# Performance work log

Hardware: AMD Instinct MI355X
Metric: run time of the kernel (lower is better)

## Reference

```python
import jax, jax.numpy as jnp
import numpy as np

N_NODES = 100000
N_EDGES = 1600000
IN_DIM, HID_DIM, LAT_DIM = 128, 128, 32


def gcn_conv(x, W, b, src, dst, ew, num_nodes):
    """PyG GCNConv with improved=True (self-loop fill value 2.0),
    symmetric normalization D^-1/2 (A + 2I) D^-1/2, then linear + bias."""
    loop = jnp.arange(num_nodes)
    src2 = jnp.concatenate([src, loop])
    dst2 = jnp.concatenate([dst, loop])
    ew2 = jnp.concatenate([ew, jnp.full((num_nodes,), 2.0, dtype=x.dtype)])
    # deg[i] = sum of incoming edge weights (incl. self loop weight 2)
    deg = jax.ops.segment_sum(ew2, dst2, num_segments=num_nodes)
    dinv = jnp.where(deg > 0, jax.lax.rsqrt(deg), 0.0)
    norm = dinv[src2] * ew2 * dinv[dst2]           # [E+N]
    h = x @ W                                      # linear first: [N, out]
    msg = h[src2] * norm[:, None]                  # gather + scale: [E+N, out]
    out = jax.ops.segment_sum(msg, dst2, num_segments=num_nodes)
    return out + b


def setup_inputs() -> dict:
    key = jax.random.key(0)
    ks = jax.random.split(key, 8)
    x = jax.random.normal(ks[0], (N_NODES, IN_DIM), dtype=jnp.float32)
    edge_index = jax.random.randint(ks[1], (2, N_EDGES), 0, N_NODES, dtype=jnp.int64)
    edge_weight = jnp.ones((N_EDGES,), dtype=jnp.float32)
    s = 1.0 / np.sqrt(IN_DIM)
    W1 = jax.random.normal(ks[2], (IN_DIM, HID_DIM), dtype=jnp.float32) * s
    b1 = jnp.zeros((HID_DIM,), dtype=jnp.float32)
    sh = 1.0 / np.sqrt(HID_DIM)
    Wm = jax.random.normal(ks[3], (HID_DIM, LAT_DIM), dtype=jnp.float32) * sh
    bm = jnp.zeros((LAT_DIM,), dtype=jnp.float32)
    Ws = jax.random.normal(ks[4], (HID_DIM, LAT_DIM), dtype=jnp.float32) * sh
    bs = jnp.zeros((LAT_DIM,), dtype=jnp.float32)
    return {"x": x, "edge_index": edge_index, "edge_weight": edge_weight,
            "W1": W1, "b1": b1, "Wm": Wm, "bm": bm, "Ws": Ws, "bs": bs}


def reference(x, edge_index, edge_weight, W1, b1, Wm, bm, Ws, bs):
    src, dst = edge_index[0], edge_index[1]
    n = x.shape[0]
    h = gcn_conv(x, W1, b1, src, dst, edge_weight, n)
    h = jax.nn.relu(h)
    z_mean = gcn_conv(h, Wm, bm, src, dst, edge_weight, n)
    z_logstd = gcn_conv(h, Ws, bs, src, dst, edge_weight, n)
    return (z_mean, z_logstd)
```

## Files before the change

### kernel.cpp

```cpp
#include <hip/hip_runtime.h>


#define DIM 128
#define LAT 32
#define SCAN_ELEMS 1024
#define CPAD 32

typedef short bf16x8 __attribute__((ext_vector_type(8)));
typedef float f32x4 __attribute__((ext_vector_type(4)));

__device__ __forceinline__ unsigned short f2bf(float f) {
    unsigned u = __float_as_uint(f);
    return (unsigned short)((u + 0x7fffu + ((u >> 16) & 1u)) >> 16);
}
__device__ __forceinline__ unsigned packbf(float a, float b) {
    return (unsigned)f2bf(a) | ((unsigned)f2bf(b) << 16);
}
__device__ __forceinline__ float2 bfp2f(unsigned u) {
    float2 r;
    r.x = __uint_as_float(u << 16);
    r.y = __uint_as_float(u & 0xffff0000u);
    return r;
}

__global__ void k_x2bf(const float* __restrict__ x, uint2* __restrict__ xb, int n4) {
    int i = blockIdx.x * blockDim.x + threadIdx.x;
    if (i < n4) {
        float4 v = reinterpret_cast<const float4*>(x)[i];
        xb[i] = make_uint2(packbf(v.x, v.y), packbf(v.z, v.w));
    }
}

__global__ void k_rank(const int* __restrict__ dst, int* __restrict__ cursorPad,
                       unsigned short* __restrict__ rank, int E) {
    int e = blockIdx.x * blockDim.x + threadIdx.x;
    if (e < E) rank[e] = (unsigned short)atomicAdd(&cursorPad[(size_t)dst[e] * CPAD], 1);
}

__global__ __launch_bounds__(256) void k_scan1(const int* __restrict__ countsPad,
                                               int* __restrict__ rowptr,
                                               int* __restrict__ bsums, int N) {
    __shared__ int sdata[256];
    const int t = threadIdx.x;
    const int base = blockIdx.x * SCAN_ELEMS + t * 4;
    int v[4];
#pragma unroll
    for (int j = 0; j < 4; ++j) {
        int idx = base + j;
        v[j] = (idx < N) ? countsPad[(size_t)idx * CPAD] : 0;
    }
    int tot = v[0] + v[1] + v[2] + v[3];
    sdata[t] = tot;
    __syncthreads();
    for (int off = 1; off < 256; off <<= 1) {
        int x = 0;
        if (t >= off) x = sdata[t - off];
        __syncthreads();
        if (t >= off) sdata[t] += x;
        __syncthreads();
    }
    int running = sdata[t] - tot;
#pragma unroll
    for (int j = 0; j < 4; ++j) {
        int idx = base + j;
        if (idx < N) rowptr[idx] = running;
        running += v[j];
    }
    if (t == 255) bsums[blockIdx.x] = sdata[255];
}

__global__ void k_scan2(int* __restrict__ bsums, int* __restrict__ rowptr, int NB, int N, int E) {
    int running = 0;
    for (int b = 0; b < NB; ++b) {
        int t = bsums[b];
        bsums[b] = running;
        running += t;
    }
    rowptr[N] = E;
}

__global__ void k_scan3(int* __restrict__ rowptr, const int* __restrict__ bsums, int N) {
    int i = blockIdx.x * blockDim.x + threadIdx.x;
    if (i < N) rowptr[i] += bsums[i >> 10];
}

__global__ void k_place(const int* __restrict__ src, const int* __restrict__ dst,
                        const float* __restrict__ ew, const unsigned short* __restrict__ rank,
                        const int* __restrict__ rowptr, int2* __restrict__ csr, int E) {
    int e = blockIdx.x * blockDim.x + threadIdx.x;
    if (e < E)
        csr[rowptr[dst[e]] + rank[e]] = make_int2(src[e], __float_as_int(ew[e]));
}

__global__ void k_degseg(const int2* __restrict__ csr, const int* __restrict__ rowptr,
                         float* __restrict__ dinv, int N) {
    int i = blockIdx.x * blockDim.x + threadIdx.x;
    if (i >= N) return;
    float deg = 2.0f;
    int p = rowptr[i], end = rowptr[i + 1];
    for (; p < end; ++p) deg += __int_as_float(csr[p].y);
    dinv[i] = (deg > 0.0f) ? rsqrtf(deg) : 0.0f;
}

__global__ void k_prep_w(const float* __restrict__ W1, const float* __restrict__ Wm,
                         const float* __restrict__ Ws, unsigned short* __restrict__ w1t,
                         unsigned short* __restrict__ wct) {
    int i = blockIdx.x * 256 + threadIdx.x;
    if (i < DIM * DIM) {
        int c = i >> 7, k = i & 127;
        w1t[c * DIM + k] = f2bf(W1[k * DIM + c]);
    }
    i -= DIM * DIM;
    if (i >= 0 && i < 64 * DIM) {
        int c = i >> 7, k = i & 127;
        wct[c * DIM + k] = f2bf((c < LAT) ? Wm[k * LAT + c] : Ws[k * LAT + (c - LAT)]);
    }
}

__global__ __launch_bounds__(256) void k_gather128(const int2* __restrict__ csr,
                                                   const int* __restrict__ rowptr,
                                                   const float* __restrict__ dinv,
                                                   const uint4* __restrict__ xb,
                                                   uint4* __restrict__ axb, int N) {
    int node = (blockIdx.x * 256 + threadIdx.x) >> 6;
    int lane = threadIdx.x & 63;
    if (node >= N) return;
    const int q = lane >> 4;
    const int l = lane & 15;
    float di = dinv[node];
    float acc[8];
#pragma unroll
    for (int j = 0; j < 8; ++j) acc[j] = 0.f;
    if (q == 0) {
        uint4 sv = xb[(size_t)node * 16 + l];
        float sl = 2.0f * di;
        float2 s0 = bfp2f(sv.x), s1 = bfp2f(sv.y), s2 = bfp2f(sv.z), s3 = bfp2f(sv.w);
        acc[0] = s0.x * sl; acc[1] = s0.y * sl;
        acc[2] = s1.x * sl; acc[3] = s1.y * sl;
        acc[4] = s2.x * sl; acc[5] = s2.y * sl;
        acc[6] = s3.x * sl; acc[7] = s3.y * sl;
    }
    int p = rowptr[node] + q;
    int end = rowptr[node + 1];
    for (; p + 4 < end; p += 8) {
        int2 e0 = csr[p];
        int2 e1 = csr[p + 4];
        float n0 = __int_as_float(e0.y) * dinv[e0.x];
        float n1 = __int_as_float(e1.y) * dinv[e1.x];
        uint4 u0 = xb[(size_t)e0.x * 16 + l];
        uint4 u1 = xb[(size_t)e1.x * 16 + l];
        float2 a0 = bfp2f(u0.x), a1 = bfp2f(u0.y), a2 = bfp2f(u0.z), a3 = bfp2f(u0.w);
        acc[0] = fmaf(a0.x, n0, acc[0]); acc[1] = fmaf(a0.y, n0, acc[1]);
        acc[2] = fmaf(a1.x, n0, acc[2]); acc[3] = fmaf(a1.y, n0, acc[3]);
        acc[4] = fmaf(a2.x, n0, acc[4]); acc[5] = fmaf(a2.y, n0, acc[5]);
        acc[6] = fmaf(a3.x, n0, acc[6]); acc[7] = fmaf(a3.y, n0, acc[7]);
        float2 b0 = bfp2f(u1.x), b1 = bfp2f(u1.y), b2 = bfp2f(u1.z), b3 = bfp2f(u1.w);
        acc[0] = fmaf(b0.x, n1, acc[0]); acc[1] = fmaf(b0.y, n1, acc[1]);
        acc[2] = fmaf(b1.x, n1, acc[2]); acc[3] = fmaf(b1.y, n1, acc[3]);
        acc[4] = fmaf(b2.x, n1, acc[4]); acc[5] = fmaf(b2.y, n1, acc[5]);
        acc[6] = fmaf(b3.x, n1, acc[6]); acc[7] = fmaf(b3.y, n1, acc[7]);
    }
    if (p < end) {
        int2 e0 = csr[p];
        float n0 = __int_as_float(e0.y) * dinv[e0.x];
        uint4 u0 = xb[(size_t)e0.x * 16 + l];
        float2 a0 = bfp2f(u0.x), a1 = bfp2f(u0.y), a2 = bfp2f(u0.z), a3 = bfp2f(u0.w);
        acc[0] = fmaf(a0.x, n0, acc[0]); acc[1] = fmaf(a0.y, n0, acc[1]);
        acc[2] = fmaf(a1.x, n0, acc[2]); acc[3] = fmaf(a1.y, n0, acc[3]);
        acc[4] = fmaf(a2.x, n0, acc[4]); acc[5] = fmaf(a2.y, n0, acc[5]);
        acc[6] = fmaf(a3.x, n0, acc[6]); acc[7] = fmaf(a3.y, n0, acc[7]);
    }
#pragma unroll
    for (int j = 0; j < 8; ++j) {
        acc[j] += __shfl_xor(acc[j], 16);
        acc[j] += __shfl_xor(acc[j], 32);
    }
    if (q == 0) {
        uint4 o;
        o.x = packbf(acc[0] * di, acc[1] * di);
        o.y = packbf(acc[2] * di, acc[3] * di);
        o.z = packbf(acc[4] * di, acc[5] * di);
        o.w = packbf(acc[6] * di, acc[7] * di);
        axb[(size_t)node * 16 + l] = o;
    }
}

__global__ __launch_bounds__(256) void k_mfma_mlp(const unsigned short* __restrict__ axb,
                                                  const unsigned short* __restrict__ w1t,
                                                  const unsigned short* __restrict__ wct,
                                                  const float* __restrict__ b1,
                                                  unsigned short* __restrict__ hwb, int N) {
    __shared__ __align__(16) unsigned short hs[4][16][136];
    const int wave = threadIdx.x >> 6;
    const int lane = threadIdx.x & 63;
    const int lrow = lane & 15;
    const int lk = lane >> 4;
    const int R0 = blockIdx.x * 64 + wave * 16;
    const bool active = (R0 < N);

    if (active) {
        f32x4 acc[8];
#pragma unroll
        for (int t = 0; t < 8; ++t) acc[t] = (f32x4){0.f, 0.f, 0.f, 0.f};
        const unsigned short* arow = axb + (size_t)(R0 + lrow) * DIM + lk * 8;
#pragma unroll
        for (int kt = 0; kt < 4; ++kt) {
            bf16x8 a = *reinterpret_cast<const bf16x8*>(arow + kt * 32);
#pragma unroll
            for (int t = 0; t < 8; ++t) {
                bf16x8 b = *reinterpret_cast<const bf16x8*>(
                    w1t + (size_t)(t * 16 + lrow) * DIM + kt * 32 + lk * 8);
                acc[t] = __builtin_amdgcn_mfma_f32_16x16x32_bf16(a, b, acc[t], 0, 0, 0);
            }
        }
#pragma unroll
        for (int t = 0; t < 8; ++t) {
#pragma unroll
            for (int r = 0; r < 4; ++r) {
                int col = t * 16 + lrow;
                float v = acc[t][r] + b1[col];
                hs[wave][lk * 4 + r][col] = f2bf(v > 0.f ? v : 0.f);
            }
        }
    }
    __syncthreads();
    if (active) {
        f32x4 acc2[4];
#pragma unroll
        for (int t = 0; t < 4; ++t) acc2[t] = (f32x4){0.f, 0.f, 0.f, 0.f};
        const unsigned short* hrow = &hs[wave][lrow][0];
#pragma unroll
        for (int kt = 0; kt < 4; ++kt) {
            bf16x8 a = *reinterpret_cast<const bf16x8*>(hrow + kt * 32 + lk * 8);
#pragma unroll
            for (int t = 0; t < 4; ++t) {
                bf16x8 b = *reinterpret_cast<const bf16x8*>(
                    wct + (size_t)(t * 16 + lrow) * DIM + kt * 32 + lk * 8);
                acc2[t] = __builtin_amdgcn_mfma_f32_16x16x32_bf16(a, b, acc2[t], 0, 0, 0);
            }
        }
#pragma unroll
        for (int t = 0; t < 4; ++t)
#pragma unroll
            for (int r = 0; r < 4; ++r)
                hwb[(size_t)(R0 + lk * 4 + r) * 64 + t * 16 + lrow] = f2bf(acc2[t][r]);
    }
}

__global__ __launch_bounds__(256) void k_gather64(const int2* __restrict__ csr,
                                                  const int* __restrict__ rowptr,
                                                  const float* __restrict__ dinv,
                                                  const uint2* __restrict__ hwb,
                                                  const float* __restrict__ bm,
                                                  const float* __restrict__ bs,
                                                  float* __restrict__ outm,
                                                  float* __restrict__ outs, int N) {
    int node = (blockIdx.x * 256 + threadIdx.x) >> 6;
    int lane = threadIdx.x & 63;
    if (node >= N) return;
    const int q = lane >> 4;
    const int l = lane & 15;
    float di = dinv[node];
    float acc[4];
#pragma unroll
    for (int j = 0; j < 4; ++j) acc[j] = 0.f;
    if (q == 0) {
        uint2 sv = hwb[(size_t)node * 16 + l];
        float sl = 2.0f * di;
        float2 s0 = bfp2f(sv.x), s1 = bfp2f(sv.y);
        acc[0] = s0.x * sl; acc[1] = s0.y * sl;
        acc[2] = s1.x * sl; acc[3] = s1.y * sl;
    }
    int p = rowptr[node] + q;
    int end = rowptr[node + 1];
    for (; p + 4 < end; p += 8) {
        int2 e0 = csr[p];
        int2 e1 = csr[p + 4];
        float n0 = __int_as_float(e0.y) * dinv[e0.x];
        float n1 = __int_as_float(e1.y) * dinv[e1.x];
        uint2 u0 = hwb[(size_t)e0.x * 16 + l];
        uint2 u1 = hwb[(size_t)e1.x * 16 + l];
        float2 a0 = bfp2f(u0.x), a1 = bfp2f(u0.y);
        float2 b0 = bfp2f(u1.x), b1 = bfp2f(u1.y);
        acc[0] = fmaf(a0.x, n0, acc[0]); acc[1] = fmaf(a0.y, n0, acc[1]);
        acc[2] = fmaf(a1.x, n0, acc[2]); acc[3] = fmaf(a1.y, n0, acc[3]);
        acc[0] = fmaf(b0.x, n1, acc[0]); acc[1] = fmaf(b0.y, n1, acc[1]);
        acc[2] = fmaf(b1.x, n1, acc[2]); acc[3] = fmaf(b1.y, n1, acc[3]);
    }
    if (p < end) {
        int2 e0 = csr[p];
        float n0 = __int_as_float(e0.y) * dinv[e0.x];
        uint2 u0 = hwb[(size_t)e0.x * 16 + l];
        float2 a0 = bfp2f(u0.x), a1 = bfp2f(u0.y);
        acc[0] = fmaf(a0.x, n0, acc[0]); acc[1] = fmaf(a0.y, n0, acc[1]);
        acc[2] = fmaf(a1.x, n0, acc[2]); acc[3] = fmaf(a1.y, n0, acc[3]);
    }
#pragma unroll
    for (int j = 0; j < 4; ++j) {
        acc[j] += __shfl_xor(acc[j], 16);
        acc[j] += __shfl_xor(acc[j], 32);
    }
    if (q == 0) {
        if (l < 8) {
            float4 bb = reinterpret_cast<const float4*>(bm)[l];
            float4 val;
            val.x = acc[0] * di + bb.x;
            val.y = acc[1] * di + bb.y;
            val.z = acc[2] * di + bb.z;
            val.w = acc[3] * di + bb.w;
            reinterpret_cast<float4*>(outm + (size_t)node * LAT)[l] = val;
        } else {
            float4 bb = reinterpret_cast<const float4*>(bs)[l - 8];
            float4 val;
            val.x = acc[0] * di + bb.x;
            val.y = acc[1] * di + bb.y;
            val.z = acc[2] * di + bb.z;
            val.w = acc[3] * di + bb.w;
            reinterpret_cast<float4*>(outs + (size_t)node * LAT)[l - 8] = val;
        }
    }
}

extern "C" void kernel_launch(void* const* d_in, const int* in_sizes, int n_in,
                              void* d_out, int out_size, void* d_ws, size_t ws_size,
                              hipStream_t stream) {
    const float* x  = (const float*)d_in[0];
    const int*   ei = (const int*)d_in[1];
    const float* ew = (const float*)d_in[2];
    const float* W1 = (const float*)d_in[3];
    const float* b1 = (const float*)d_in[4];
    const float* Wm = (const float*)d_in[5];
    const float* bm = (const float*)d_in[6];
    const float* Ws = (const float*)d_in[7];
    const float* bs = (const float*)d_in[8];

    const int N = in_sizes[0] / DIM;
    const int E = in_sizes[1] / 2;
    const int* src = ei;
    const int* dst = ei + E;

    char* w = (char*)d_ws;
    unsigned* xb  = (unsigned*)w;            w += (size_t)N * DIM * 2;
    unsigned* axb = (unsigned*)w;            w += (size_t)N * DIM * 2;
    unsigned short* hwb = (unsigned short*)w; w += (size_t)N * 64 * 2;
    float* dinv = (float*)w;                 w += (size_t)N * 4;
    int*   rowptr = (int*)w;                 w += (size_t)(N + 1) * 4;
    unsigned short* rank = (unsigned short*)w; w += (size_t)E * 2;
    w = (char*)(((size_t)w + 255) & ~(size_t)255);
    int*   bsums  = (int*)w;                 w += 1024 * 4;
    unsigned short* w1t = (unsigned short*)w; w += DIM * DIM * 2;
    unsigned short* wct = (unsigned short*)w; w += 64 * DIM * 2;
    w = (char*)(((size_t)w + 255) & ~(size_t)255);
    int*   cursorPad = (int*)w;              w += (size_t)N * CPAD * 4;
    w = (char*)(((size_t)w + 255) & ~(size_t)255);
    int2*  csr    = (int2*)w;

    float* outm = (float*)d_out;
    float* outs = outm + (size_t)N * LAT;

    const int B = 256;
    const int NB = (N + SCAN_ELEMS - 1) / SCAN_ELEMS;

    hipMemsetAsync(cursorPad, 0, (size_t)N * CPAD * 4, stream);
    k_rank<<<(E + B - 1) / B, B, 0, stream>>>(dst, cursorPad, rank, E);
    k_x2bf<<<((N * DIM / 4) + B - 1) / B, B, 0, stream>>>(x, (uint2*)xb, N * DIM / 4);
    k_prep_w<<<(DIM * DIM + 64 * DIM + B - 1) / B, B, 0, stream>>>(W1, Wm, Ws, w1t, wct);

    k_scan1<<<NB, B, 0, stream>>>(cursorPad, rowptr, bsums, N);
    k_scan2<<<1, 1, 0, stream>>>(bsums, rowptr, NB, N, E);
    k_scan3<<<(N + B - 1) / B, B, 0, stream>>>(rowptr, bsums, N);
    k_place<<<(E + B - 1) / B, B, 0, stream>>>(src, dst, ew, rank, rowptr, csr, E);
    k_degseg<<<(N + B - 1) / B, B, 0, stream>>>(csr, rowptr, dinv, N);

    k_gather128<<<(N + 3) / 4, B, 0, stream>>>(csr, rowptr, dinv, (const uint4*)xb, (uint4*)axb, N);

    k_mfma_mlp<<<(N + 63) / 64, B, 0, stream>>>((const unsigned short*)axb, w1t, wct, b1, hwb, N);

    k_gather64<<<(N + 3) / 4, B, 0, stream>>>(csr, rowptr, dinv, (const uint2*)hwb, bm, bs, outm, outs, N);
}
```

Baseline: 307.2 us.

## Fuse prep kernels, drop padded cursor, merge scan passes, unroll gathers deeper

Merges the rank atomics, x-to-bf16 conversion and weight prep into one launch, with the atomic pass vectorized over four edges per thread. The cursor array loses its 32-int padding, which shrinks the memset and the scan read but lets atomics on different destinations share cache lines. The two scan follow-up kernels collapse into one where each block sums the preceding block totals serially. Both gather kernels now unroll four edges per iteration instead of two, to raise memory-level parallelism on the random row loads.

```diff
diff --git a/kernel.cpp b/kernel.cpp
--- a/kernel.cpp
+++ b/kernel.cpp
@@ -4,7 +4,6 @@
 #define DIM 128
 #define LAT 32
 #define SCAN_ELEMS 1024
-#define CPAD 32
 
 typedef short bf16x8 __attribute__((ext_vector_type(8)));
 typedef float f32x4 __attribute__((ext_vector_type(4)));
@@ -23,21 +22,58 @@
     return r;
 }
 
-__global__ void k_x2bf(const float* __restrict__ x, uint2* __restrict__ xb, int n4) {
-    int i = blockIdx.x * blockDim.x + threadIdx.x;
-    if (i < n4) {
-        float4 v = reinterpret_cast<const float4*>(x)[i];
-        xb[i] = make_uint2(packbf(v.x, v.y), packbf(v.z, v.w));
-    }
-}
-
-__global__ void k_rank(const int* __restrict__ dst, int* __restrict__ cursorPad,
-                       unsigned short* __restrict__ rank, int E) {
-    int e = blockIdx.x * blockDim.x + threadIdx.x;
-    if (e < E) rank[e] = (unsigned short)atomicAdd(&cursorPad[(size_t)dst[e] * CPAD], 1);
-}
-
-__global__ __launch_bounds__(256) void k_scan1(const int* __restrict__ countsPad,
+__global__ __launch_bounds__(256) void k_prep(const int* __restrict__ dst,
+                                              int* __restrict__ cursor,
+                                              unsigned short* __restrict__ rank, int E,
+                                              const float* __restrict__ x,
+                                              uint4* __restrict__ xb,
+                                              const float* __restrict__ W1,
+                                              const float* __restrict__ Wm,
+                                              const float* __restrict__ Ws,
+                                              unsigned short* __restrict__ w1t,
+                                              unsigned short* __restrict__ wct,
+                                              int RB, int XB) {
+    const int b = blockIdx.x;
+    if (b < RB) {
+        int idx = b * 1024 + threadIdx.x * 4;
+        if (idx + 3 < E) {
+            int4 d4 = *reinterpret_cast<const int4*>(dst + idx);
+            unsigned short r0 = (unsigned short)atomicAdd(&cursor[d4.x], 1);
+            unsigned short r1 = (unsigned short)atomicAdd(&cursor[d4.y], 1);
+            unsigned short r2 = (unsigned short)atomicAdd(&cursor[d4.z], 1);
+            unsigned short r3 = (unsigned short)atomicAdd(&cursor[d4.w], 1);
+            ushort4 r = {r0, r1, r2, r3};
+            *reinterpret_cast<ushort4*>(rank + idx) = r;
+        } else {
+            for (int j = 0; j < 4 && idx + j < E; ++j)
+                rank[idx + j] = (unsigned short)atomicAdd(&cursor[dst[idx + j]], 1);
+        }
+    } else if (b < RB + XB) {
+        size_t i = ((size_t)(b - RB) * 256 + threadIdx.x) * 16;
+        const float4* xin = reinterpret_cast<const float4*>(x + i);
+        float4 v0 = xin[0], v1 = xin[1], v2 = xin[2], v3 = xin[3];
+        uint4 o0, o1;
+        o0.x = packbf(v0.x, v0.y); o0.y = packbf(v0.z, v0.w);
+        o0.z = packbf(v1.x, v1.y); o0.w = packbf(v1.z, v1.w);
+        o1.x = packbf(v2.x, v2.y); o1.y = packbf(v2.z, v2.w);
+        o1.z = packbf(v3.x, v3.y); o1.w = packbf(v3.z, v3.w);
+        xb[i / 8] = o0;
+        xb[i / 8 + 1] = o1;
+    } else {
+        int i = (b - RB - XB) * 256 + threadIdx.x;
+        if (i < DIM * DIM) {
+            int c = i >> 7, k = i & 127;
+            w1t[c * DIM + k] = f2bf(W1[k * DIM + c]);
+        }
+        i -= DIM * DIM;
+        if (i >= 0 && i < 64 * DIM) {
+            int c = i >> 7, k = i & 127;
+            wct[c * DIM + k] = f2bf((c < LAT) ? Wm[k * LAT + c] : Ws[k * LAT + (c - LAT)]);
+        }
+    }
+}
+
+__global__ __launch_bounds__(256) void k_scan1(const int* __restrict__ counts,
                                                int* __restrict__ rowptr,
                                                int* __restrict__ bsums, int N) {
     __shared__ int sdata[256];
@@ -47,7 +83,7 @@
 #pragma unroll
     for (int j = 0; j < 4; ++j) {
         int idx = base + j;
-        v[j] = (idx < N) ? countsPad[(size_t)idx * CPAD] : 0;
+        v[j] = (idx < N) ? counts[idx] : 0;
     }
     int tot = v[0] + v[1] + v[2] + v[3];
     sdata[t] = tot;
@@ -69,19 +105,24 @@
     if (t == 255) bsums[blockIdx.x] = sdata[255];
 }
 
-__global__ void k_scan2(int* __restrict__ bsums, int* __restrict__ rowptr, int NB, int N, int E) {
-    int running = 0;
-    for (int b = 0; b < NB; ++b) {
-        int t = bsums[b];
-        bsums[b] = running;
-        running += t;
-    }
-    rowptr[N] = E;
-}
-
-__global__ void k_scan3(int* __restrict__ rowptr, const int* __restrict__ bsums, int N) {
-    int i = blockIdx.x * blockDim.x + threadIdx.x;
-    if (i < N) rowptr[i] += bsums[i >> 10];
+__global__ __launch_bounds__(256) void k_scanfix(int* __restrict__ rowptr,
+                                                 const int* __restrict__ bsums,
+                                                 int N, int E) {
+    __shared__ int pfx;
+    if (threadIdx.x == 0) {
+        int s = 0;
+        for (int j = 0; j < (int)blockIdx.x; ++j) s += bsums[j];
+        pfx = s;
+        if (blockIdx.x == 0) rowptr[N] = E;
+    }
+    __syncthreads();
+    int s = pfx;
+    int base = blockIdx.x * SCAN_ELEMS + threadIdx.x * 4;
+#pragma unroll
+    for (int j = 0; j < 4; ++j) {
+        int idx = base + j;
+        if (idx < N) rowptr[idx] += s;
+    }
 }
 
 __global__ void k_place(const int* __restrict__ src, const int* __restrict__ dst,
@@ -100,21 +141,6 @@
     int p = rowptr[i], end = rowptr[i + 1];
     for (; p < end; ++p) deg += __int_as_float(csr[p].y);
     dinv[i] = (deg > 0.0f) ? rsqrtf(deg) : 0.0f;
-}
-
-__global__ void k_prep_w(const float* __restrict__ W1, const float* __restrict__ Wm,
-                         const float* __restrict__ Ws, unsigned short* __restrict__ w1t,
-                         unsigned short* __restrict__ wct) {
-    int i = blockIdx.x * 256 + threadIdx.x;
-    if (i < DIM * DIM) {
-        int c = i >> 7, k = i & 127;
-        w1t[c * DIM + k] = f2bf(W1[k * DIM + c]);
-    }
-    i -= DIM * DIM;
-    if (i >= 0 && i < 64 * DIM) {
-        int c = i >> 7, k = i & 127;
-        wct[c * DIM + k] = f2bf((c < LAT) ? Wm[k * LAT + c] : Ws[k * LAT + (c - LAT)]);
-    }
 }
 
 __global__ __launch_bounds__(256) void k_gather128(const int2* __restrict__ csr,
@@ -142,25 +168,46 @@
     }
     int p = rowptr[node] + q;
     int end = rowptr[node + 1];
-    for (; p + 4 < end; p += 8) {
-        int2 e0 = csr[p];
-        int2 e1 = csr[p + 4];
+    for (; p + 12 < end; p += 16) {
+        int2 e0 = csr[p], e1 = csr[p + 4], e2 = csr[p + 8], e3 = csr[p + 12];
         float n0 = __int_as_float(e0.y) * dinv[e0.x];
         float n1 = __int_as_float(e1.y) * dinv[e1.x];
+        float n2 = __int_as_float(e2.y) * dinv[e2.x];
+        float n3 = __int_as_float(e3.y) * dinv[e3.x];
         uint4 u0 = xb[(size_t)e0.x * 16 + l];
         uint4 u1 = xb[(size_t)e1.x * 16 + l];
-        float2 a0 = bfp2f(u0.x), a1 = bfp2f(u0.y), a2 = bfp2f(u0.z), a3 = bfp2f(u0.w);
-        acc[0] = fmaf(a0.x, n0, acc[0]); acc[1] = fmaf(a0.y, n0, acc[1]);
-        acc[2] = fmaf(a1.x, n0, acc[2]); acc[3] = fmaf(a1.y, n0, acc[3]);
-        acc[4] = fmaf(a2.x, n0, acc[4]); acc[5] = fmaf(a2.y, n0, acc[5]);
-        acc[6] = fmaf(a3.x, n0, acc[6]); acc[7] = fmaf(a3.y, n0, acc[7]);
-        float2 b0 = bfp2f(u1.x), b1 = bfp2f(u1.y), b2 = bfp2f(u1.z), b3 = bfp2f(u1.w);
-        acc[0] = fmaf(b0.x, n1, acc[0]); acc[1] = fmaf(b0.y, n1, acc[1]);
-        acc[2] = fmaf(b1.x, n1, acc[2]); acc[3] = fmaf(b1.y, n1, acc[3]);
-        acc[4] = fmaf(b2.x, n1, acc[4]); acc[5] = fmaf(b2.y, n1, acc[5]);
-        acc[6] = fmaf(b3.x, n1, acc[6]); acc[7] = fmaf(b3.y, n1, acc[7]);
-    }
-    if (p < end) {
+        uint4 u2 = xb[(size_t)e2.x * 16 + l];
+        uint4 u3 = xb[(size_t)e3.x * 16 + l];
+        {
+            float2 a0 = bfp2f(u0.x), a1 = bfp2f(u0.y), a2 = bfp2f(u0.z), a3 = bfp2f(u0.w);
+            acc[0] = fmaf(a0.x, n0, acc[0]); acc[1] = fmaf(a0.y, n0, acc[1]);
+            acc[2] = fmaf(a1.x, n0, acc[2]); acc[3] = fmaf(a1.y, n0, acc[3]);
+            acc[4] = fmaf(a2.x, n0, acc[4]); acc[5] = fmaf(a2.y, n0, acc[5]);
+            acc[6] = fmaf(a3.x, n0, acc[6]); acc[7] = fmaf(a3.y, n0, acc[7]);
+        }
+        {
+            float2 a0 = bfp2f(u1.x), a1 = bfp2f(u1.y), a2 = bfp2f(u1.z), a3 = bfp2f(u1.w);
+            acc[0] = fmaf(a0.x, n1, acc[0]); acc[1] = fmaf(a0.y, n1, acc[1]);
+            acc[2] = fmaf(a1.x, n1, acc[2]); acc[3] = fmaf(a1.y, n1, acc[3]);
+            acc[4] = fmaf(a2.x, n1, acc[4]); acc[5] = fmaf(a2.y, n1, acc[5]);
+            acc[6] = fmaf(a3.x, n1, acc[6]); acc[7] = fmaf(a3.y, n1, acc[7]);
+        }
+        {
+            float2 a0 = bfp2f(u2.x), a1 = bfp2f(u2.y), a2 = bfp2f(u2.z), a3 = bfp2f(u2.w);
+            acc[0] = fmaf(a0.x, n2, acc[0]); acc[1] = fmaf(a0.y, n2, acc[1]);
+            acc[2] = fmaf(a1.x, n2, acc[2]); acc[3] = fmaf(a1.y, n2, acc[3]);
+            acc[4] = fmaf(a2.x, n2, acc[4]); acc[5] = fmaf(a2.y, n2, acc[5]);
+            acc[6] = fmaf(a3.x, n2, acc[6]); acc[7] = fmaf(a3.y, n2, acc[7]);
+        }
+        {
+            float2 a0 = bfp2f(u3.x), a1 = bfp2f(u3.y), a2 = bfp2f(u3.z), a3 = bfp2f(u3.w);
+            acc[0] = fmaf(a0.x, n3, acc[0]); acc[1] = fmaf(a0.y, n3, acc[1]);
+            acc[2] = fmaf(a1.x, n3, acc[2]); acc[3] = fmaf(a1.y, n3, acc[3]);
+            acc[4] = fmaf(a2.x, n3, acc[4]); acc[5] = fmaf(a2.y, n3, acc[5]);
+            acc[6] = fmaf(a3.x, n3, acc[6]); acc[7] = fmaf(a3.y, n3, acc[7]);
+        }
+    }
+    for (; p < end; p += 4) {
         int2 e0 = csr[p];
         float n0 = __int_as_float(e0.y) * dinv[e0.x];
         uint4 u0 = xb[(size_t)e0.x * 16 + l];
@@ -273,21 +320,30 @@
     }
     int p = rowptr[node] + q;
     int end = rowptr[node + 1];
-    for (; p + 4 < end; p += 8) {
-        int2 e0 = csr[p];
-        int2 e1 = csr[p + 4];
+    for (; p + 12 < end; p += 16) {
+        int2 e0 = csr[p], e1 = csr[p + 4], e2 = csr[p + 8], e3 = csr[p + 12];
         float n0 = __int_as_float(e0.y) * dinv[e0.x];
         float n1 = __int_as_float(e1.y) * dinv[e1.x];
+        float n2 = __int_as_float(e2.y) * dinv[e2.x];
+        float n3 = __int_as_float(e3.y) * dinv[e3.x];
         uint2 u0 = hwb[(size_t)e0.x * 16 + l];
         uint2 u1 = hwb[(size_t)e1.x * 16 + l];
+        uint2 u2 = hwb[(size_t)e2.x * 16 + l];
+        uint2 u3 = hwb[(size_t)e3.x * 16 + l];
         float2 a0 = bfp2f(u0.x), a1 = bfp2f(u0.y);
-        float2 b0 = bfp2f(u1.x), b1 = bfp2f(u1.y);
         acc[0] = fmaf(a0.x, n0, acc[0]); acc[1] = fmaf(a0.y, n0, acc[1]);
         acc[2] = fmaf(a1.x, n0, acc[2]); acc[3] = fmaf(a1.y, n0, acc[3]);
+        float2 b0 = bfp2f(u1.x), b1 = bfp2f(u1.y);
         acc[0] = fmaf(b0.x, n1, acc[0]); acc[1] = fmaf(b0.y, n1, acc[1]);
         acc[2] = fmaf(b1.x, n1, acc[2]); acc[3] = fmaf(b1.y, n1, acc[3]);
-    }
-    if (p < end) {
+        float2 c0 = bfp2f(u2.x), c1 = bfp2f(u2.y);
+        acc[0] = fmaf(c0.x, n2, acc[0]); acc[1] = fmaf(c0.y, n2, acc[1]);
+        acc[2] = fmaf(c1.x, n2, acc[2]); acc[3] = fmaf(c1.y, n2, acc[3]);
+        float2 d0 = bfp2f(u3.x), d1 = bfp2f(u3.y);
+        acc[0] = fmaf(d0.x, n3, acc[0]); acc[1] = fmaf(d0.y, n3, acc[1]);
+        acc[2] = fmaf(d1.x, n3, acc[2]); acc[3] = fmaf(d1.y, n3, acc[3]);
+    }
+    for (; p < end; p += 4) {
         int2 e0 = csr[p];
         float n0 = __int_as_float(e0.y) * dinv[e0.x];
         uint2 u0 = hwb[(size_t)e0.x * 16 + l];
@@ -344,6 +400,7 @@
     unsigned* axb = (unsigned*)w;            w += (size_t)N * DIM * 2;
     unsigned short* hwb = (unsigned short*)w; w += (size_t)N * 64 * 2;
     float* dinv = (float*)w;                 w += (size_t)N * 4;
+    int*   cursor = (int*)w;                 w += (size_t)N * 4;
     int*   rowptr = (int*)w;                 w += (size_t)(N + 1) * 4;
     unsigned short* rank = (unsigned short*)w; w += (size_t)E * 2;
     w = (char*)(((size_t)w + 255) & ~(size_t)255);
@@ -351,8 +408,6 @@
     unsigned short* w1t = (unsigned short*)w; w += DIM * DIM * 2;
     unsigned short* wct = (unsigned short*)w; w += 64 * DIM * 2;
     w = (char*)(((size_t)w + 255) & ~(size_t)255);
-    int*   cursorPad = (int*)w;              w += (size_t)N * CPAD * 4;
-    w = (char*)(((size_t)w + 255) & ~(size_t)255);
     int2*  csr    = (int2*)w;
 
     float* outm = (float*)d_out;
@@ -360,15 +415,16 @@
 
     const int B = 256;
     const int NB = (N + SCAN_ELEMS - 1) / SCAN_ELEMS;
-
-    hipMemsetAsync(cursorPad, 0, (size_t)N * CPAD * 4, stream);
-    k_rank<<<(E + B - 1) / B, B, 0, stream>>>(dst, cursorPad, rank, E);
-    k_x2bf<<<((N * DIM / 4) + B - 1) / B, B, 0, stream>>>(x, (uint2*)xb, N * DIM / 4);
-    k_prep_w<<<(DIM * DIM + 64 * DIM + B - 1) / B, B, 0, stream>>>(W1, Wm, Ws, w1t, wct);
-
-    k_scan1<<<NB, B, 0, stream>>>(cursorPad, rowptr, bsums, N);
-    k_scan2<<<1, 1, 0, stream>>>(bsums, rowptr, NB, N, E);
-    k_scan3<<<(N + B - 1) / B, B, 0, stream>>>(rowptr, bsums, N);
+    const int RB = (E + 1023) / 1024;
+    const int XB = (N * DIM / 16) / 256;
+    const int WB = (DIM * DIM + 64 * DIM) / 256;
+
+    hipMemsetAsync(cursor, 0, (size_t)N * 4, stream);
+    k_prep<<<RB + XB + WB, B, 0, stream>>>(dst, cursor, rank, E, x, (uint4*)xb,
+                                           W1, Wm, Ws, w1t, wct, RB, XB);
+
+    k_scan1<<<NB, B, 0, stream>>>(cursor, rowptr, bsums, N);
+    k_scanfix<<<NB, B, 0, stream>>>(rowptr, bsums, N, E);
     k_place<<<(E + B - 1) / B, B, 0, stream>>>(src, dst, ew, rank, rowptr, csr, E);
     k_degseg<<<(N + B - 1) / B, B, 0, stream>>>(csr, rowptr, dinv, N);
 
```

After: 305.7 us. About the same (-0.5%).
